# Kernel tuning notes

Measured on AMD Instinct MI355X. Metric: run time of the kernel, lower is better.

Reference implementation:

```python
import jax, jax.numpy as jnp
import numpy as np

FRONT, END = 1, 2            # COMBINE_FRONT / COMBINE_END label values
BOS_ID, EOS_ID = 0, 1
BS, SLEN, D, H, L = 16, 256, 1024, 16, 2
N_POS = 512                  # N_MAX_POSITIONS


def setup_inputs():
    key = jax.random.key(0)
    ks = iter(jax.random.split(key, 80))
    nrm = lambda shape: jax.random.normal(next(ks), shape, dtype=jnp.float32) * 0.02
    inp = {}
    inp["encoded"] = jax.random.normal(next(ks), (BS, SLEN, D), dtype=jnp.float32)
    inp["lengths"] = jnp.full((BS,), SLEN, dtype=jnp.int32)  # assert slen == lengths.max()
    # deterministic valid word-span labels: [F,F,F,E,O,F,E,O] repeated -> words of 4 and 2 subwords
    pat = np.tile(np.array([1, 1, 1, 2, 0, 1, 2, 0], dtype=np.int32), SLEN // 8)
    inp["combine_labels"] = jnp.asarray(np.broadcast_to(pat, (BS, SLEN)).copy())
    inp["lang_id"] = 0
    inp["pos_emb"] = nrm((N_POS, D))
    inp["special_emb"] = nrm((3, D)).at[2].set(0.0)  # padding_idx=2 row zeroed
    for p in ("ctx", "wc"):
        for w in ("Wq", "Wk", "Wv", "Wo"):
            inp[p + "_" + w] = nrm((L, D, D))
        for b in ("bq", "bk", "bv", "bo", "b2", "be1", "be2"):
            inp[p + "_" + b] = jnp.zeros((L, D), dtype=jnp.float32)
        inp[p + "_W1"] = nrm((L, D, 4 * D))
        inp[p + "_b1"] = jnp.zeros((L, 4 * D), dtype=jnp.float32)
        inp[p + "_W2"] = nrm((L, 4 * D, D))
        inp[p + "_g1"] = jnp.ones((L, D), dtype=jnp.float32)
        inp[p + "_g2"] = jnp.ones((L, D), dtype=jnp.float32)
    return inp


def _ln(x, g, b):
    m = x.mean(-1, keepdims=True)
    v = ((x - m) ** 2).mean(-1, keepdims=True)
    return (x - m) / jnp.sqrt(v + 1e-5) * g + b


def _encoder(x, pad, P):
    # post-norm TransformerEncoder (torch default): attn -> add&LN -> relu-FFN -> add&LN
    Wq, Wk, Wv, Wo, bq, bk, bv, bo, W1, b1, W2, b2, g1, be1, g2, be2 = P
    B, S, Dm = x.shape
    hd = Dm // H
    scale = 1.0 / np.sqrt(hd)
    for i in range(Wq.shape[0]):
        q = (x @ Wq[i] + bq[i]).reshape(B, S, H, hd)
        k = (x @ Wk[i] + bk[i]).reshape(B, S, H, hd)
        v = (x @ Wv[i] + bv[i]).reshape(B, S, H, hd)
        s = jnp.einsum("bqhd,bkhd->bhqk", q, k) * scale
        s = jnp.where(pad[:, None, None, :], -1e9, s)  # src_key_padding_mask
        a = jax.nn.softmax(s, axis=-1)
        o = jnp.einsum("bhqk,bkhd->bqhd", a, v).reshape(B, S, Dm) @ Wo[i] + bo[i]
        x = _ln(x + o, g1[i], be1[i])
        h = jax.nn.relu(x @ W1[i] + b1[i]) @ W2[i] + b2[i]
        x = _ln(x + h, g2[i], be2[i])
    return x


def _word_inputs(encoded, combine_labels, special_emb):
    # vectorized replacement of the nested python-loop ragged span builder;
    # index math on the (concrete) labels in numpy, gathers/scatters in jnp.
    cl = np.asarray(combine_labels)
    f = cl == FRONT
    e = cl == END
    c = np.cumsum(f.astype(np.int64), axis=1)
    frontrun = c - np.maximum.accumulate(np.where(f, 0, c), axis=1)  # run of FRONTs ending here
    fr_prev = np.pad(frontrun[:, :-1], ((0, 0), (1, 0)))
    slot = np.where(f, frontrun, fr_prev + 1)  # 1-based slot inside word (slot 0 = BOS)
    e_flat = e.reshape(-1)
    wid = np.cumsum(e_flat) - e_flat  # word id = #ENDs strictly before, row-major order
    tok_idx = np.nonzero((f | e).reshape(-1))[0]
    w_tok = wid[tok_idx]
    s_tok = slot.reshape(-1)[tok_idx]
    wlen = fr_prev[e] + 3  # k subwords (fr_prev+1) + BOS + EOS
    n_word = wlen.shape[0]
    maxL = int(wlen.max())
    Dm = encoded.shape[-1]
    x = jnp.zeros((n_word, maxL, Dm), dtype=encoded.dtype)
    x = x.at[:, 0].set(special_emb[BOS_ID])
    x = x.at[np.arange(n_word), wlen - 1].set(special_emb[EOS_ID])  # eos at slot k+1
    x = x.at[w_tok, s_tok].set(encoded.reshape(-1, Dm)[tok_idx])
    return x, wlen


def _forward(encoded, lengths, combine_labels, pos_emb, special_emb, ctx, wc):
    S = encoded.shape[1]
    pad = jnp.asarray(np.arange(S)[None, :] >= np.asarray(lengths)[:, None])
    x = _encoder(encoded + pos_emb[:S][None], pad, ctx)          # another_encode
    winp, wlen = _word_inputs(x, combine_labels, special_emb)    # ragged gather, [n_word, maxL, D]
    maxL = winp.shape[1]
    wpad = jnp.asarray(np.arange(maxL)[None, :] >= wlen[:, None])
    y = _encoder(winp + pos_emb[:maxL][None], wpad, wc)          # word_encode
    return y[:, 0]  # position-0 (BOS) representation, [n_word, D]


def reference(encoded, lengths, combine_labels, lang_id, pos_emb, special_emb,
              ctx_Wq, ctx_Wk, ctx_Wv, ctx_Wo, ctx_bq, ctx_bk, ctx_bv, ctx_bo,
              ctx_W1, ctx_b1, ctx_W2, ctx_b2, ctx_g1, ctx_be1, ctx_g2, ctx_be2,
              wc_Wq, wc_Wk, wc_Wv, wc_Wo, wc_bq, wc_bk, wc_bv, wc_bo,
              wc_W1, wc_b1, wc_W2, wc_b2, wc_g1, wc_be1, wc_g2, wc_be2):
    ctx = (ctx_Wq, ctx_Wk, ctx_Wv, ctx_Wo, ctx_bq, ctx_bk, ctx_bv, ctx_bo,
           ctx_W1, ctx_b1, ctx_W2, ctx_b2, ctx_g1, ctx_be1, ctx_g2, ctx_be2)
    wc = (wc_Wq, wc_Wk, wc_Wv, wc_Wo, wc_bq, wc_bk, wc_bv, wc_bo,
          wc_W1, wc_b1, wc_W2, wc_b2, wc_g1, wc_be1, wc_g2, wc_be2)
    return _forward(encoded, lengths, combine_labels, pos_emb, special_emb, ctx, wc)
```

## Files before the change

kernel.cpp:

```cpp
#include <hip/hip_runtime.h>
#include <stdint.h>

typedef unsigned short u16;
typedef __attribute__((ext_vector_type(8))) short short8;
typedef __attribute__((ext_vector_type(4))) short short4v;
typedef __attribute__((ext_vector_type(4))) float f32x4;

#define DEV static __device__ __forceinline__

constexpr int B = 16, S = 256, D = 1024, H = 16, LYR = 2, FF = 4096;
constexpr int Mc = B * S;
constexpr int MAXL = 6;
constexpr int QKVS = 3 * D;

DEV u16 f2b(float f) {
  union { float f; uint32_t u; } a; a.f = f;
  uint32_t r = a.u + 0x7fffu + ((a.u >> 16) & 1u);
  return (u16)(r >> 16);
}
DEV float b2f(u16 b) {
  union { uint32_t u; float f; } a; a.u = ((uint32_t)b) << 16;
  return a.f;
}

DEV void glds16(const u16* g, u16* l) {
  __builtin_amdgcn_global_load_lds((const __attribute__((address_space(1))) void*)g,
                                   (__attribute__((address_space(3))) void*)l, 16, 0, 0);
}

struct TBatch {
  const float* src[6];
  u16* dst[6];
  int Kd[6];
  int Nd[6];
  int base[6];
};

__global__ __launch_bounds__(256) void transpose_batch(TBatch tb, int unused) {
  __shared__ float tile[32][33];
  const int bid = blockIdx.x;
  int wi = 0;
#pragma unroll
  for (int i = 1; i < 6; i++)
    if (bid >= tb.base[i]) wi = i;
  const float* __restrict__ W = tb.src[wi];
  u16* __restrict__ Wt = tb.dst[wi];
  const int K = tb.Kd[wi], N = tb.Nd[wi];
  const int local = bid - tb.base[wi];
  const int ntx = N >> 5;
  const int bn = (local % ntx) * 32, bk = (local / ntx) * 32;
  const int t = threadIdx.x, tx = t & 31, ty = t >> 5;
#pragma unroll
  for (int i = 0; i < 32; i += 8)
    tile[ty + i][tx] = W[(size_t)(bk + ty + i) * N + bn + tx];
  __syncthreads();
#pragma unroll
  for (int i = 0; i < 32; i += 8)
    Wt[(size_t)(bn + ty + i) * K + bk + tx] = f2b(tile[tx][ty + i]);
}


template <int PASSES>
DEV void stage_rows(const u16* P, int lda, int k0, u16* Dst, int t) {
#pragma unroll
  for (int p = 0; p < PASSES; p++)
    glds16(P + (size_t)(p * 32) * lda + k0, Dst + p * 2048 + t * 8);
}

DEV void compute_tile(const u16* Asb, const u16* Bsb, f32x4 (&acc)[4][8],
                      int wm, int wn, int li, int hi) {
#pragma unroll
  for (int ks = 0; ks < 2; ks++) {
    const int ch = ((((ks << 2) | hi) ^ (li & 7)) * 8);
    short8 af[4], bfr[8];
#pragma unroll
    for (int i = 0; i < 4; i++)
      af[i] = *(const short8*)&Asb[(wm + i * 16 + li) * 64 + ch];
#pragma unroll
    for (int j = 0; j < 8; j++)
      bfr[j] = *(const short8*)&Bsb[(wn + j * 16 + li) * 64 + ch];
#pragma unroll
    for (int i = 0; i < 4; i++)
#pragma unroll
      for (int j = 0; j < 8; j++)
        acc[i][j] = __builtin_amdgcn_mfma_f32_16x16x32_bf16(af[i], bfr[j], acc[i][j], 0, 0, 0);
  }
}

template <int EPI, bool SPLITB, bool SPLITK>
__global__ __launch_bounds__(256, 2) void gemm_bt(const u16* __restrict__ A,
                                                  const u16* __restrict__ Bt,
                                                  const float* __restrict__ bias0,
                                                  const float* __restrict__ bias1,
                                                  const float* __restrict__ bias2,
                                                  float* __restrict__ Cf, u16* __restrict__ Cb,
                                                  int M, int N, int K, int lda, int NB) {
  __shared__ u16 As[128 * 64];
  __shared__ u16 Bs[256 * 64];
  const int t = threadIdx.x, lane = t & 63, w = t >> 6;
  const int wm = (w >> 1) * 64, wn = (w & 1) * 128;
  const int nwg = gridDim.x;
  const int cpx = nwg >> 3;
  const int swz = (blockIdx.x & 7) * cpx + (blockIdx.x >> 3);
  int sblk = 0, rem = swz;
  if (SPLITK) {
    const int tps = nwg >> 1;
    sblk = (swz >= tps) ? 1 : 0;
    rem = swz - sblk * tps;
  }
  const int n0 = (rem % NB) * 256, m0 = (rem / NB) * 128;
  const int pr = t >> 3;
  const int scb = (((t & 7) ^ (pr & 7)) * 8);
  f32x4 acc[4][8] = {};
  const u16* Ap = A + (size_t)sblk * K + (size_t)(m0 + pr) * lda + scb;
  const u16* Bp = Bt + (size_t)sblk * K + (size_t)(n0 + pr) * lda + scb;
  const int li = lane & 15, hi = lane >> 4;

  for (int k0 = 0; k0 < K; k0 += 64) {
    stage_rows<4>(Ap, lda, k0, &As[0], t);
    stage_rows<8>(Bp, lda, k0, &Bs[0], t);
    __syncthreads();
    compute_tile(&As[0], &Bs[0], acc, wm, wn, li, hi);
    __syncthreads();
  }

  float* Cfs = Cf;
  if (SPLITK && EPI == 3) Cfs = Cf + (size_t)sblk * M * N;
  const int rg = hi * 4;
#pragma unroll
  for (int j = 0; j < 8; j++) {
    const int col = n0 + wn + j * 16 + li;
    float bv = 0.f;
    if (EPI != 3)
      bv = SPLITB ? (col < 1024 ? bias0 : col < 2048 ? bias1 : bias2)[col & 1023]
                  : bias0[col];
#pragma unroll
    for (int i = 0; i < 4; i++) {
      const int row0 = m0 + wm + i * 16 + rg;
#pragma unroll
      for (int r = 0; r < 4; r++) {
        float v = acc[i][j][r] + bv;
        if (EPI == 2) v = fmaxf(v, 0.f);
        if (EPI == 0 || EPI == 3) Cfs[(size_t)(row0 + r) * N + col] = v;
        else Cb[(size_t)(row0 + r) * N + col] = f2b(v);
      }
    }
  }
}

__global__ __launch_bounds__(256) void transpose_v(const u16* __restrict__ QKV,
                                                   u16* __restrict__ Vt) {
  const int kb = blockIdx.x, h = blockIdx.y, b = blockIdx.z;
  __shared__ u16 tile[64][72];
  const int t = threadIdx.x, lr = t >> 3, lc = (t & 7) * 8;
#pragma unroll
  for (int p = 0; p < 2; p++) {
    int r = lr + p * 32;
    *(short8*)&tile[r][lc] =
        *(const short8*)&QKV[(size_t)(b * 256 + kb * 64 + r) * QKVS + 2048 + h * 64 + lc];
  }
  __syncthreads();
#pragma unroll
  for (int p = 0; p < 2; p++) {
    int hd = lr + p * 32;
    short8 v8;
#pragma unroll
    for (int j = 0; j < 8; j++) v8[j] = (short)tile[lc + j][hd];
    *(short8*)&Vt[(size_t)((b * 16 + h) * 64 + hd) * 256 + kb * 64 + lc] = v8;
  }
}

__global__ __launch_bounds__(256) void attn_ctx(const u16* __restrict__ QKV,
                                                const u16* __restrict__ Vt,
                                                u16* __restrict__ AO,
                                                const int* __restrict__ lengths) {
  const int qt = blockIdx.x, h = blockIdx.y, b = blockIdx.z;
  __shared__ u16 Qs[64 * 64], Ks[64 * 64], Vs[64 * 64], Ps[64 * 64];
  const int t = threadIdx.x, lane = t & 63, w = t >> 6;
  const int len = lengths[b];
  const int lr = t >> 3, lc = (t & 7) * 8;
#pragma unroll
  for (int p = 0; p < 2; p++) {
    int r = lr + p * 32;
    *(short8*)&Qs[r * 64 + lc] =
        *(const short8*)&QKV[(size_t)(b * 256 + qt * 64 + r) * QKVS + h * 64 + lc];
  }
  const int li = lane & 15, kk = (lane >> 4) * 8, rg = (lane >> 4) * 4;
  float mrun[4], lrun[4];
  f32x4 oacc[4] = {};
#pragma unroll
  for (int r = 0; r < 4; r++) { mrun[r] = -1e30f; lrun[r] = 0.f; }

  for (int kt = 0; kt < 4; kt++) {
    __syncthreads();
#pragma unroll
    for (int p = 0; p < 2; p++) {
      int r = lr + p * 32;
      *(short8*)&Ks[r * 64 + lc] =
          *(const short8*)&QKV[(size_t)(b * 256 + kt * 64 + r) * QKVS + 1024 + h * 64 + lc];
      *(short8*)&Vs[r * 64 + lc] =
          *(const short8*)&Vt[(size_t)((b * 16 + h) * 64 + r) * 256 + kt * 64 + lc];
    }
    __syncthreads();
    f32x4 s[4] = {};
    short8 aq0 = *(const short8*)&Qs[(w * 16 + li) * 64 + kk];
    short8 aq1 = *(const short8*)&Qs[(w * 16 + li) * 64 + 32 + kk];
#pragma unroll
    for (int fn = 0; fn < 4; fn++) {
      short8 b0 = *(const short8*)&Ks[(fn * 16 + li) * 64 + kk];
      short8 b1 = *(const short8*)&Ks[(fn * 16 + li) * 64 + 32 + kk];
      s[fn] = __builtin_amdgcn_mfma_f32_16x16x32_bf16(aq0, b0, s[fn], 0, 0, 0);
      s[fn] = __builtin_amdgcn_mfma_f32_16x16x32_bf16(aq1, b1, s[fn], 0, 0, 0);
    }
    float pv[4][4];
#pragma unroll
    for (int r = 0; r < 4; r++) {
      float mx = -1e30f;
#pragma unroll
      for (int fn = 0; fn < 4; fn++) {
        int key = kt * 64 + fn * 16 + li;
        float v = (key < len) ? s[fn][r] * 0.125f : -1e30f;
        pv[fn][r] = v;
        mx = fmaxf(mx, v);
      }
#pragma unroll
      for (int d = 1; d < 16; d <<= 1) mx = fmaxf(mx, __shfl_xor(mx, d));
      float mnew = fmaxf(mrun[r], mx);
      float sf = __expf(mrun[r] - mnew);
      mrun[r] = mnew;
      float rs = 0.f;
#pragma unroll
      for (int fn = 0; fn < 4; fn++) {
        int key = kt * 64 + fn * 16 + li;
        float p = (key < len) ? __expf(pv[fn][r] - mnew) : 0.f;
        pv[fn][r] = p;
        rs += p;
      }
#pragma unroll
      for (int d = 1; d < 16; d <<= 1) rs += __shfl_xor(rs, d);
      lrun[r] = lrun[r] * sf + rs;
#pragma unroll
      for (int fn = 0; fn < 4; fn++) oacc[fn][r] *= sf;
    }
#pragma unroll
    for (int fn = 0; fn < 4; fn++)
#pragma unroll
      for (int r = 0; r < 4; r++)
        Ps[(w * 16 + rg + r) * 64 + fn * 16 + li] = f2b(pv[fn][r]);
#pragma unroll
    for (int ks = 0; ks < 2; ks++) {
      short8 ap = *(const short8*)&Ps[(w * 16 + li) * 64 + ks * 32 + kk];
#pragma unroll
      for (int fn = 0; fn < 4; fn++) {
        short8 bv = *(const short8*)&Vs[(fn * 16 + li) * 64 + ks * 32 + kk];
        oacc[fn] = __builtin_amdgcn_mfma_f32_16x16x32_bf16(ap, bv, oacc[fn], 0, 0, 0);
      }
    }
  }
#pragma unroll
  for (int r = 0; r < 4; r++) {
    float inv = 1.f / fmaxf(lrun[r], 1e-30f);
    int row = b * 256 + qt * 64 + w * 16 + rg + r;
#pragma unroll
    for (int fn = 0; fn < 4; fn++) {
      int col = h * 64 + fn * 16 + li;
      AO[(size_t)row * 1024 + col] = f2b(oacc[fn][r] * inv);
    }
  }
}

__global__ __launch_bounds__(256) void attn_word(const u16* __restrict__ QKV,
                                                 const int* __restrict__ wlen,
                                                 u16* __restrict__ AO, int NW) {
  const int idx = blockIdx.x * 256 + threadIdx.x;
  if (idx >= NW * 16 * MAXL) return;
  const int i = idx % MAXL, h = (idx / MAXL) % 16, wd = idx / (MAXL * 16);
  const int len = wlen[wd];
  const size_t rowb = (size_t)(wd * MAXL + i) * QKVS;
  float q[64];
#pragma unroll
  for (int d = 0; d < 64; d += 8) {
    short8 q8 = *(const short8*)&QKV[rowb + h * 64 + d];
#pragma unroll
    for (int e = 0; e < 8; e++) q[d + e] = b2f((u16)q8[e]);
  }
  float sc[MAXL];
  float mx = -1e30f;
  for (int j = 0; j < MAXL; j++) {
    if (j >= len) { sc[j] = -1e30f; continue; }
    const size_t koff = (size_t)(wd * MAXL + j) * QKVS + 1024 + h * 64;
    float dot = 0.f;
#pragma unroll
    for (int d = 0; d < 64; d += 8) {
      short8 k8 = *(const short8*)&QKV[koff + d];
#pragma unroll
      for (int e = 0; e < 8; e++) dot += q[d + e] * b2f((u16)k8[e]);
    }
    sc[j] = dot * 0.125f;
    mx = fmaxf(mx, sc[j]);
  }
  float p[MAXL], l = 0.f;
  for (int j = 0; j < MAXL; j++) {
    p[j] = (j < len) ? __expf(sc[j] - mx) : 0.f;
    l += p[j];
  }
  const float rl = 1.f / fmaxf(l, 1e-30f);
  for (int j = 0; j < MAXL; j++) p[j] *= rl;
#pragma unroll
  for (int d = 0; d < 64; d += 8) {
    float acc[8] = {};
    for (int j = 0; j < MAXL; j++) {
      if (j >= len) break;
      short8 v8 = *(const short8*)&QKV[(size_t)(wd * MAXL + j) * QKVS + 2048 + h * 64 + d];
#pragma unroll
      for (int e = 0; e < 8; e++) acc[e] += p[j] * b2f((u16)v8[e]);
    }
    short8 o8;
#pragma unroll
    for (int e = 0; e < 8; e++) o8[e] = (short)f2b(acc[e]);
    *(short8*)&AO[(size_t)(wd * MAXL + i) * 1024 + h * 64 + d] = o8;
  }
}

__global__ __launch_bounds__(256) void ln_resid2(const float* __restrict__ X,
                                                 const float* __restrict__ P0,
                                                 const float* __restrict__ P1,
                                                 const float* __restrict__ bias,
                                                 const float* __restrict__ g,
                                                 const float* __restrict__ be,
                                                 float* __restrict__ Xo, u16* __restrict__ Xb) {
  const int row = blockIdx.x, t = threadIdx.x;
  const size_t base = (size_t)row * 1024 + t * 4;
  float4 x4 = *(const float4*)&X[base];
  float4 p0 = *(const float4*)&P0[base];
  float4 p1 = *(const float4*)&P1[base];
  float4 bb = *(const float4*)&bias[t * 4];
  float v[4] = { x4.x + p0.x + p1.x + bb.x, x4.y + p0.y + p1.y + bb.y,
                 x4.z + p0.z + p1.z + bb.z, x4.w + p0.w + p1.w + bb.w };
  float s = v[0] + v[1] + v[2] + v[3];
  float q = v[0] * v[0] + v[1] * v[1] + v[2] * v[2] + v[3] * v[3];
#pragma unroll
  for (int d = 1; d < 64; d <<= 1) { s += __shfl_xor(s, d); q += __shfl_xor(q, d); }
  __shared__ float ss[4], qq[4];
  if ((t & 63) == 0) { ss[t >> 6] = s; qq[t >> 6] = q; }
  __syncthreads();
  s = ss[0] + ss[1] + ss[2] + ss[3];
  q = qq[0] + qq[1] + qq[2] + qq[3];
  const float mean = s * (1.f / 1024.f);
  const float var = q * (1.f / 1024.f) - mean * mean;
  const float rstd = rsqrtf(var + 1e-5f);
  float4 gv = *(const float4*)&g[t * 4];
  float4 bv = *(const float4*)&be[t * 4];
  float y[4];
  y[0] = (v[0] - mean) * rstd * gv.x + bv.x;
  y[1] = (v[1] - mean) * rstd * gv.y + bv.y;
  y[2] = (v[2] - mean) * rstd * gv.z + bv.z;
  y[3] = (v[3] - mean) * rstd * gv.w + bv.w;
  *(float4*)&Xo[base] = make_float4(y[0], y[1], y[2], y[3]);
  short4v o = { (short)f2b(y[0]), (short)f2b(y[1]), (short)f2b(y[2]), (short)f2b(y[3]) };
  *(short4v*)&Xb[base] = o;
}

__global__ __launch_bounds__(256) void posadd(const float* __restrict__ enc,
                                              const float* __restrict__ pos,
                                              float* __restrict__ X, u16* __restrict__ Xb) {
  const int row = blockIdx.x, t = threadIdx.x;
  const int sp = row & 255;
  const size_t base = (size_t)row * 1024 + t * 4;
  float4 e = *(const float4*)&enc[base];
  float4 p = *(const float4*)&pos[(size_t)sp * 1024 + t * 4];
  float y[4] = { e.x + p.x, e.y + p.y, e.z + p.z, e.w + p.w };
  *(float4*)&X[base] = make_float4(y[0], y[1], y[2], y[3]);
  short4v o = { (short)f2b(y[0]), (short)f2b(y[1]), (short)f2b(y[2]), (short)f2b(y[3]) };
  *(short4v*)&Xb[base] = o;
}

__global__ void scan_words(const int* __restrict__ labels, int* __restrict__ t2w,
                           int* __restrict__ t2s, int* __restrict__ wlen) {
  __shared__ int rowEnds[16], rowBase[16];
  const int t = threadIdx.x;
  if (t < 16) {
    int c = 0;
    for (int s = 0; s < 256; s++) c += (labels[t * 256 + s] == 2);
    rowEnds[t] = c;
  }
  __syncthreads();
  if (t == 0) {
    int acc = 0;
    for (int b2 = 0; b2 < 16; b2++) { rowBase[b2] = acc; acc += rowEnds[b2]; }
  }
  __syncthreads();
  if (t < 16) {
    int wc = rowBase[t], fr = 0;
    for (int s = 0; s < 256; s++) {
      const int tok = t * 256 + s, lb = labels[tok];
      if (lb == 1) { fr++; t2w[tok] = wc; t2s[tok] = fr; }
      else if (lb == 2) { t2w[tok] = wc; t2s[tok] = fr + 1; wlen[wc] = fr + 3; wc++; fr = 0; }
      else { t2w[tok] = -1; t2s[tok] = 0; fr = 0; }
    }
  }
}

__global__ __launch_bounds__(256) void build_winp(const float* __restrict__ pos,
                                                  const float* __restrict__ spec,
                                                  const int* __restrict__ wlen,
                                                  float* __restrict__ XW) {
  const int row = blockIdx.x;
  const int wd = row / MAXL, sl = row % MAXL;
  const int len = wlen[wd];
  const int t = threadIdx.x;
  const size_t cb = t * 4;
  float4 p = *(const float4*)&pos[(size_t)sl * 1024 + cb];
  float4 e = make_float4(0.f, 0.f, 0.f, 0.f);
  if (sl == 0) e = *(const float4*)&spec[cb];
  else if (sl == len - 1) e = *(const float4*)&spec[1024 + cb];
  *(float4*)&XW[(size_t)row * 1024 + cb] =
      make_float4(p.x + e.x, p.y + e.y, p.z + e.z, p.w + e.w);
}

__global__ __launch_bounds__(256) void scatter_tokens(const float* __restrict__ Xc,
                                                      const int* __restrict__ t2w,
                                                      const int* __restrict__ t2s,
                                                      float* __restrict__ XW) {
  const int tok = blockIdx.x;
  const int wd = t2w[tok];
  if (wd < 0) return;
  const int row = wd * MAXL + t2s[tok];
  const size_t cb = threadIdx.x * 4;
  float4 a = *(const float4*)&Xc[(size_t)tok * 1024 + cb];
  float* dst = &XW[(size_t)row * 1024 + cb];
  float4 b2 = *(const float4*)dst;
  *(float4*)dst = make_float4(a.x + b2.x, a.y + b2.y, a.z + b2.z, a.w + b2.w);
}

__global__ __launch_bounds__(256) void to_bf16_k(const float* __restrict__ X,
                                                 u16* __restrict__ Xb) {
  const size_t base = (size_t)blockIdx.x * 1024 + threadIdx.x * 4;
  float4 v = *(const float4*)&X[base];
  short4v o = { (short)f2b(v.x), (short)f2b(v.y), (short)f2b(v.z), (short)f2b(v.w) };
  *(short4v*)&Xb[base] = o;
}

__global__ __launch_bounds__(256) void gather_out(const float* __restrict__ XW,
                                                  float* __restrict__ out) {
  const int wd = blockIdx.x;
  const size_t cb = threadIdx.x * 4;
  *(float4*)&out[(size_t)wd * 1024 + cb] =
      *(const float4*)&XW[(size_t)(wd * MAXL) * 1024 + cb];
}

extern "C" void kernel_launch(void* const* d_in, const int* in_sizes, int n_in,
                              void* d_out, int out_size, void* d_ws, size_t ws_size,
                              hipStream_t stream) {
  const float* encoded = (const float*)d_in[0];
  const int* lengths = (const int*)d_in[1];
  const int* labels = (const int*)d_in[2];
  const float* pos = (const float*)d_in[4];
  const float* spec = (const float*)d_in[5];
  const float* W[2][16];
  for (int p = 0; p < 2; p++)
    for (int i = 0; i < 16; i++) W[p][i] = (const float*)d_in[6 + p * 16 + i];

  const int NW = out_size / D;
  const int Mw = NW * MAXL;

  char* wp = (char*)d_ws;
  size_t off = 0;
  auto alloc = [&](size_t bytes) {
    void* r = wp + off;
    off += (bytes + 255) & ~(size_t)255;
    return r;
  };
  float* x_ctx = (float*)alloc((size_t)Mc * D * 4);
  float* x_word = (float*)alloc((size_t)Mw * D * 4);
  u16* xb = (u16*)alloc((size_t)Mw * D * 2);
  u16* wtQKV = (u16*)alloc((size_t)3 * D * D * 2);
  u16* wtO = (u16*)alloc((size_t)D * D * 2);
  u16* wtW1 = (u16*)alloc((size_t)D * FF * 2);
  u16* wtW2 = (u16*)alloc((size_t)D * FF * 2);
  char* uni = (char*)alloc((size_t)Mw * FF * 2);
  u16* QKV = (u16*)uni;
  u16* Vt = (u16*)(uni + ((size_t)40 << 20));
  u16* hb = (u16*)uni;
  u16* AOb = (u16*)alloc((size_t)Mw * D * 2);
  float* tmp = (float*)alloc((size_t)2 * Mw * D * 4);
  int* t2w = (int*)alloc((size_t)Mc * 4);
  int* t2s = (int*)alloc((size_t)Mc * 4);
  int* wlen = (int*)alloc((size_t)NW * 4);
  (void)ws_size; (void)in_sizes; (void)n_in;

  posadd<<<Mc, 256, 0, stream>>>(encoded, pos, x_ctx, xb);

  auto run_encoder = [&](int p, float* X, int M, bool is_ctx) {
    for (int l = 0; l < LYR; l++) {
      const size_t oDD = (size_t)l * D * D, oDF = (size_t)l * D * FF;
      TBatch tb;
      tb.src[0] = W[p][0] + oDD; tb.dst[0] = wtQKV;               tb.Kd[0] = D;  tb.Nd[0] = D;
      tb.src[1] = W[p][1] + oDD; tb.dst[1] = wtQKV + (size_t)D * D;   tb.Kd[1] = D;  tb.Nd[1] = D;
      tb.src[2] = W[p][2] + oDD; tb.dst[2] = wtQKV + (size_t)2 * D * D; tb.Kd[2] = D; tb.Nd[2] = D;
      tb.src[3] = W[p][3] + oDD; tb.dst[3] = wtO;                 tb.Kd[3] = D;  tb.Nd[3] = D;
      tb.src[4] = W[p][11] + oDF; tb.dst[4] = wtW1;               tb.Kd[4] = D;  tb.Nd[4] = FF;
      tb.src[5] = W[p][13] + oDF; tb.dst[5] = wtW2;               tb.Kd[5] = FF; tb.Nd[5] = D;
      int base = 0;
      for (int i = 0; i < 6; i++) {
        tb.base[i] = base;
        base += (tb.Kd[i] / 32) * (tb.Nd[i] / 32);
      }
      transpose_batch<<<base, 256, 0, stream>>>(tb, 0);

      gemm_bt<1, true, false><<<(3 * D / 256) * (M / 128), 256, 0, stream>>>(
          xb, wtQKV, W[p][4] + (size_t)l * D, W[p][5] + (size_t)l * D,
          W[p][6] + (size_t)l * D, nullptr, QKV, M, 3 * D, D, D, 3 * D / 256);
      if (is_ctx) {
        transpose_v<<<dim3(4, H, B), 256, 0, stream>>>(QKV, Vt);
        attn_ctx<<<dim3(4, H, B), 256, 0, stream>>>(QKV, Vt, AOb, lengths);
      } else {
        attn_word<<<(NW * H * MAXL + 255) / 256, 256, 0, stream>>>(QKV, wlen, AOb, NW);
      }
      gemm_bt<3, false, true><<<2 * (D / 256) * (M / 128), 256, 0, stream>>>(
          AOb, wtO, nullptr, nullptr, nullptr, tmp, nullptr, M, D, 512, D, D / 256);
      ln_resid2<<<M, 256, 0, stream>>>(X, tmp, tmp + (size_t)M * D, W[p][7] + (size_t)l * D,
                                       W[p][14] + (size_t)l * D, W[p][9] + (size_t)l * D, X, xb);
      gemm_bt<2, false, false><<<(FF / 256) * (M / 128), 256, 0, stream>>>(
          xb, wtW1, W[p][12] + (size_t)l * FF, nullptr, nullptr, nullptr, hb, M, FF, D, D,
          FF / 256);
      gemm_bt<3, false, true><<<2 * (D / 256) * (M / 128), 256, 0, stream>>>(
          hb, wtW2, nullptr, nullptr, nullptr, tmp, nullptr, M, D, 2048, FF, D / 256);
      ln_resid2<<<M, 256, 0, stream>>>(X, tmp, tmp + (size_t)M * D, W[p][8] + (size_t)l * D,
                                       W[p][15] + (size_t)l * D, W[p][10] + (size_t)l * D, X, xb);
    }
  };

  run_encoder(0, x_ctx, Mc, true);

  scan_words<<<1, 64, 0, stream>>>(labels, t2w, t2s, wlen);
  build_winp<<<Mw, 256, 0, stream>>>(pos, spec, wlen, x_word);
  scatter_tokens<<<Mc, 256, 0, stream>>>(x_ctx, t2w, t2s, x_word);
  to_bf16_k<<<Mw, 256, 0, stream>>>(x_word, xb);

  run_encoder(1, x_word, Mw, false);

  gather_out<<<NW, 256, 0, stream>>>(x_word, (float*)d_out);
}
```

Baseline: 1.042 ms.

## Double-buffer GEMM LDS tiles and widen weight transpose to 64x64 vector tiles

The GEMM main loop now uses two LDS buffers and prefetches the next K tile with global_load_lds while the current one is computed, using explicit vmcnt waits and raw barriers in place of a load-sync-compute-sync loop. This is meant to hide global memory latency behind MFMA work. LDS use doubles to 96KB and the occupancy hint of 2 blocks is dropped, so fewer blocks may be resident per CU. The weight transpose kernel also moves to 64x64 tiles with float4 loads and 16-byte bf16 stores to cut memory transactions.

After: 1.281 ms. 22.9% more time.

```diff
diff --git a/kernel.cpp b/kernel.cpp
--- a/kernel.cpp
+++ b/kernel.cpp
@@ -7,6 +7,7 @@
 typedef __attribute__((ext_vector_type(4))) float f32x4;
 
 #define DEV static __device__ __forceinline__
+#define WAITVM(N) asm volatile("s_waitcnt vmcnt(" #N ")" ::: "memory")
 
 constexpr int B = 16, S = 256, D = 1024, H = 16, LYR = 2, FF = 4096;
 constexpr int Mc = B * S;
@@ -37,7 +38,7 @@
 };
 
 __global__ __launch_bounds__(256) void transpose_batch(TBatch tb, int unused) {
-  __shared__ float tile[32][33];
+  __shared__ float tile[64][65];
   const int bid = blockIdx.x;
   int wi = 0;
 #pragma unroll
@@ -47,16 +48,25 @@
   u16* __restrict__ Wt = tb.dst[wi];
   const int K = tb.Kd[wi], N = tb.Nd[wi];
   const int local = bid - tb.base[wi];
-  const int ntx = N >> 5;
-  const int bn = (local % ntx) * 32, bk = (local / ntx) * 32;
-  const int t = threadIdx.x, tx = t & 31, ty = t >> 5;
-#pragma unroll
-  for (int i = 0; i < 32; i += 8)
-    tile[ty + i][tx] = W[(size_t)(bk + ty + i) * N + bn + tx];
+  const int ntx = N >> 6;
+  const int bn = (local % ntx) * 64, bk = (local / ntx) * 64;
+  const int t = threadIdx.x;
+  const int lr = t >> 2, lc = (t & 3) * 16;
+#pragma unroll
+  for (int q = 0; q < 4; q++) {
+    float4 v = *(const float4*)&W[(size_t)(bk + lr) * N + bn + lc + q * 4];
+    *(float4*)&tile[lr][lc + q * 4] = v;
+  }
   __syncthreads();
-#pragma unroll
-  for (int i = 0; i < 32; i += 8)
-    Wt[(size_t)(bn + ty + i) * K + bk + tx] = f2b(tile[tx][ty + i]);
+  const int k0 = (t & 7) * 8;
+#pragma unroll
+  for (int p = 0; p < 2; p++) {
+    const int n = (t >> 3) + p * 32;
+    short8 o;
+#pragma unroll
+    for (int j = 0; j < 8; j++) o[j] = (short)f2b(tile[k0 + j][n]);
+    *(short8*)&Wt[(size_t)(bn + n) * K + bk + k0] = o;
+  }
 }
 
 
@@ -88,15 +98,15 @@
 }
 
 template <int EPI, bool SPLITB, bool SPLITK>
-__global__ __launch_bounds__(256, 2) void gemm_bt(const u16* __restrict__ A,
-                                                  const u16* __restrict__ Bt,
-                                                  const float* __restrict__ bias0,
-                                                  const float* __restrict__ bias1,
-                                                  const float* __restrict__ bias2,
-                                                  float* __restrict__ Cf, u16* __restrict__ Cb,
-                                                  int M, int N, int K, int lda, int NB) {
-  __shared__ u16 As[128 * 64];
-  __shared__ u16 Bs[256 * 64];
+__global__ __launch_bounds__(256) void gemm_bt(const u16* __restrict__ A,
+                                               const u16* __restrict__ Bt,
+                                               const float* __restrict__ bias0,
+                                               const float* __restrict__ bias1,
+                                               const float* __restrict__ bias2,
+                                               float* __restrict__ Cf, u16* __restrict__ Cb,
+                                               int M, int N, int K, int lda, int NB) {
+  __shared__ u16 As[2][128 * 64];
+  __shared__ u16 Bs[2][256 * 64];
   const int t = threadIdx.x, lane = t & 63, w = t >> 6;
   const int wm = (w >> 1) * 64, wn = (w & 1) * 128;
   const int nwg = gridDim.x;
@@ -116,12 +126,40 @@
   const u16* Bp = Bt + (size_t)sblk * K + (size_t)(n0 + pr) * lda + scb;
   const int li = lane & 15, hi = lane >> 4;
 
-  for (int k0 = 0; k0 < K; k0 += 64) {
-    stage_rows<4>(Ap, lda, k0, &As[0], t);
-    stage_rows<8>(Bp, lda, k0, &Bs[0], t);
-    __syncthreads();
-    compute_tile(&As[0], &Bs[0], acc, wm, wn, li, hi);
-    __syncthreads();
+  const int nt = K >> 6;
+  stage_rows<4>(Ap, lda, 0, &As[0][0], t);
+  stage_rows<8>(Bp, lda, 0, &Bs[0][0], t);
+  stage_rows<4>(Ap, lda, 64, &As[1][0], t);
+  stage_rows<8>(Bp, lda, 64, &Bs[1][0], t);
+  WAITVM(12);
+  __builtin_amdgcn_s_barrier();
+  __builtin_amdgcn_sched_barrier(0);
+
+  for (int kt = 0; kt < nt; kt += 2) {
+    compute_tile(&As[0][0], &Bs[0][0], acc, wm, wn, li, hi);
+    __builtin_amdgcn_s_barrier();
+    __builtin_amdgcn_sched_barrier(0);
+    if (kt + 2 < nt) {
+      stage_rows<4>(Ap, lda, (kt + 2) << 6, &As[0][0], t);
+      stage_rows<8>(Bp, lda, (kt + 2) << 6, &Bs[0][0], t);
+      WAITVM(12);
+    } else {
+      WAITVM(0);
+    }
+    __builtin_amdgcn_s_barrier();
+    __builtin_amdgcn_sched_barrier(0);
+    compute_tile(&As[1][0], &Bs[1][0], acc, wm, wn, li, hi);
+    __builtin_amdgcn_s_barrier();
+    __builtin_amdgcn_sched_barrier(0);
+    if (kt + 3 < nt) {
+      stage_rows<4>(Ap, lda, (kt + 3) << 6, &As[1][0], t);
+      stage_rows<8>(Bp, lda, (kt + 3) << 6, &Bs[1][0], t);
+      WAITVM(12);
+    } else {
+      WAITVM(0);
+    }
+    __builtin_amdgcn_s_barrier();
+    __builtin_amdgcn_sched_barrier(0);
   }
 
   float* Cfs = Cf;
@@ -504,7 +542,7 @@
       int base = 0;
       for (int i = 0; i < 6; i++) {
         tb.base[i] = base;
-        base += (tb.Kd[i] / 32) * (tb.Nd[i] / 32);
+        base += (tb.Kd[i] / 64) * (tb.Nd[i] / 64);
       }
       transpose_batch<<<base, 256, 0, stream>>>(tb, 0);
 
```
